# Performance work log

Hardware: AMD Instinct MI355X
Metric: run time of the kernel (lower is better)

The kernel has to match this reference:

```python
import jax, jax.numpy as jnp
import numpy as np

# dims
B, C, H, W = 2, 256, 128, 256
P, G = 9, 8            # num_pts, num_groups
GC = C // G            # group_channels


def setup_inputs() -> dict:
    key = jax.random.key(0)
    ks = jax.random.split(key, 8)
    s = 0.02
    return {
        "feats1": jax.random.normal(ks[0], (B, C, H, W), jnp.float32),
        "feats2": jax.random.normal(ks[1], (B, C, H, W), jnp.float32),
        "anchor_points": jax.random.uniform(ks[2], (B, H * W, 2), jnp.float32),
        "norm1_g": jnp.ones((C,), jnp.float32), "norm1_b": jnp.zeros((C,), jnp.float32),
        "norm2_g": jnp.ones((C,), jnp.float32), "norm2_b": jnp.zeros((C,), jnp.float32),
        "Wv": jax.random.normal(ks[3], (C, C), jnp.float32) * s, "bv": jnp.zeros((C,), jnp.float32),
        "Ww": jax.random.normal(ks[4], (C, G * P), jnp.float32) * s, "bw": jnp.zeros((G * P,), jnp.float32),
        "Wk": jax.random.normal(ks[5], (C, P), jnp.float32) * s, "bk": jnp.zeros((P,), jnp.float32),
        "Wo": jax.random.normal(ks[6], (C, C), jnp.float32) * s, "bo": jnp.zeros((C,), jnp.float32),
    }


def _ln(x, g, b):
    # LayerNorm over the last (channel) axis, eps as torch default
    m = jnp.mean(x, axis=-1, keepdims=True)
    v = jnp.mean(jnp.square(x - m), axis=-1, keepdims=True)
    return (x - m) * jax.lax.rsqrt(v + 1e-5) * g + b


def _bilinear_sample(value, pts):
    # value: (b, H, W, C); pts: (b, N, 2) normalized [0,1] (x, y)
    # grid_sample semantics: align_corners=False, zero padding
    b, h, w, c = value.shape
    x = pts[..., 0] * w - 0.5
    y = pts[..., 1] * h - 0.5
    x0 = jnp.floor(x)
    y0 = jnp.floor(y)
    wx = (x - x0)[..., None]
    wy = (y - y0)[..., None]
    x0i = x0.astype(jnp.int32)
    y0i = y0.astype(jnp.int32)
    vflat = value.reshape(b, h * w, c)

    def gather(yi, xi):
        valid = (yi >= 0) & (yi < h) & (xi >= 0) & (xi < w)
        idx = jnp.clip(yi, 0, h - 1) * w + jnp.clip(xi, 0, w - 1)
        g = jnp.take_along_axis(vflat, idx[..., None], axis=1)
        return g * valid[..., None].astype(value.dtype)

    v00 = gather(y0i, x0i)
    v01 = gather(y0i, x0i + 1)
    v10 = gather(y0i + 1, x0i)
    v11 = gather(y0i + 1, x0i + 1)
    return (v00 * (1 - wx) * (1 - wy) + v01 * wx * (1 - wy)
            + v10 * (1 - wx) * wy + v11 * wx * wy)


def reference(feats1, feats2, anchor_points, norm1_g, norm1_b, norm2_g, norm2_b,
              Wv, bv, Ww, bw, Wk, bk, Wo, bo):
    b, c, h, w = feats1.shape
    hw = h * w
    # to_3d(dim=2): (b, c, h, w) -> (b, hw, c); LayerNorm over c
    x1 = _ln(feats1.reshape(b, c, hw).transpose(0, 2, 1), norm1_g, norm1_b)
    x2 = _ln(feats2.reshape(b, c, hw).transpose(0, 2, 1), norm2_g, norm2_b)

    # value_proj (1x1 conv == per-pixel linear)
    value = (x2 @ Wv + bv).reshape(b, h, w, c)

    # weight_proj -> (b, hw, P, G); channel layout p*G + g; softmax over the P points per group
    logits = (x1 @ Ww + bw).reshape(b, hw, P, G)
    wts = jax.nn.softmax(logits, axis=2)

    # 1D key-point generator: per-pixel learned offsets along x around the anchor
    off = x1 @ Wk + bk                                   # (b, hw, P) normalized offsets
    kx = anchor_points[..., 0:1] + off                   # (b, hw, P)
    ky = jnp.broadcast_to(anchor_points[..., 1:2], kx.shape)
    kp = jnp.stack([kx, ky], axis=-1)                    # (b, hw, P, 2)

    # deformable aggregation: bilinear gather + group-weighted sum over points
    samp = _bilinear_sample(value, kp.reshape(b, hw * P, 2)).reshape(b, hw, P, G, GC)
    agg = jnp.einsum('bnpgc,bnpg->bngc', samp, wts).reshape(b, hw, c)

    out = (agg @ Wo + bo).reshape(b, h, w, c).transpose(0, 3, 1, 2)  # (b, c, h, w)
    return out, kp.reshape(b, h, w, P, 2)
```

## Files before the change

### kernel.cpp

```cpp
#include <hip/hip_runtime.h>
#include <hip/hip_bf16.h>


constexpr int B = 2, C = 256, H = 128, W = 256;
constexpr int HW = H * W;
constexpr int P = 9, G = 8;
constexpr int PIX = 32;
constexpr int NPIX = B * HW;
constexpr int NBKT = 2 * 129;

typedef __attribute__((ext_vector_type(8))) __bf16 bf16x8;
typedef __attribute__((ext_vector_type(4))) float f32x4;
typedef __attribute__((ext_vector_type(2))) float f32x2;
typedef __attribute__((ext_vector_type(2))) __fp16 fp16x2;

static __device__ __forceinline__ unsigned short f2bf(float x) {
    __hip_bfloat16 h = __float2bfloat16(x);
    return *reinterpret_cast<unsigned short*>(&h);
}
static __device__ __forceinline__ unsigned int pack2(float a, float b) {
    return (unsigned int)f2bf(a) | ((unsigned int)f2bf(b) << 16);
}
static __device__ __forceinline__ unsigned int pkh(float a, float b) {
    fp16x2 h = __builtin_amdgcn_cvt_pkrtz(a, b);
    return *reinterpret_cast<unsigned int*>(&h);
}
static __device__ __forceinline__ float bf2f(unsigned short u) {
    return __uint_as_float((unsigned int)u << 16);
}
static __device__ __forceinline__ bf16x8 ldb8g(const unsigned short* p) {
    return *reinterpret_cast<const bf16x8*>(p);
}

#define FMA_LO(acc, pk, c) \
    asm("v_fma_mix_f32 %0, %1, %2, %0 op_sel:[0,0,0] op_sel_hi:[1,0,0]" \
        : "+v"(acc) : "v"(pk), "v"(c))
#define FMA_HI(acc, pk, c) \
    asm("v_fma_mix_f32 %0, %1, %2, %0 op_sel:[1,0,0] op_sel_hi:[1,0,0]" \
        : "+v"(acc) : "v"(pk), "v"(c))

__global__ __launch_bounds__(256) void k_prep(
    const float* __restrict__ Ww, const float* __restrict__ Wv,
    const float* __restrict__ Wo,
    unsigned short* __restrict__ WwT, unsigned short* __restrict__ WvT,
    unsigned short* __restrict__ WoT)
{
    int tid = blockIdx.x * 256 + threadIdx.x;
    if (tid < 20480) {
        int n = tid >> 8, k = tid & 255;
        WwT[tid] = f2bf((n < 72) ? Ww[k * 72 + n] : 0.f);
    } else if (tid < 20480 + 65536) {
        int i = tid - 20480;
        int n = i >> 8, k = i & 255;
        WvT[i] = f2bf(Wv[k * 256 + n]);
    } else {
        int i = tid - 86016;
        int n = i >> 8, k = i & 255;
        WoT[i] = f2bf(Wo[k * 256 + n]);
    }
}

static __device__ __forceinline__ int bucket_of(const float* anchor, int pix) {
    float ay = anchor[(size_t)pix * 2 + 1];
    int y0 = (int)floorf(ay * (float)H - 0.5f);
    y0 = min(max(y0, -1), H - 1);
    return (pix >> 15) * 129 + y0 + 1;
}

__global__ __launch_bounds__(1024) void k_hist(
    const float* __restrict__ anchor, int* __restrict__ hist64)
{
    __shared__ int h[NBKT];
    const int t = threadIdx.x, blk = blockIdx.x;
    for (int i = t; i < NBKT; i += 1024) h[i] = 0;
    __syncthreads();
    atomicAdd(&h[bucket_of(anchor, blk * 1024 + t)], 1);
    __syncthreads();
    for (int i = t; i < NBKT; i += 1024) hist64[blk * NBKT + i] = h[i];
}

__global__ __launch_bounds__(256) void k_scan(
    const int* __restrict__ hist64, int* __restrict__ off)
{
    __shared__ int tot[NBKT], base[NBKT];
    const int t = threadIdx.x;
    for (int bkt = t; bkt < NBKT; bkt += 256) {
        int run = 0;
        for (int blk = 0; blk < 64; ++blk) run += hist64[blk * NBKT + bkt];
        tot[bkt] = run;
    }
    __syncthreads();
    if (t == 0) {
        int run = 0;
        for (int i = 0; i < NBKT; ++i) { base[i] = run; run += tot[i]; }
    }
    __syncthreads();
    for (int bkt = t; bkt < NBKT; bkt += 256) {
        int run = base[bkt];
        for (int blk = 0; blk < 64; ++blk) {
            int v = hist64[blk * NBKT + bkt];
            off[blk * NBKT + bkt] = run;
            run += v;
        }
    }
}

__global__ __launch_bounds__(1024) void k_scatter(
    const float* __restrict__ anchor, const int* __restrict__ off,
    int* __restrict__ perm)
{
    __shared__ int cur[NBKT];
    const int t = threadIdx.x, blk = blockIdx.x;
    for (int i = t; i < NBKT; i += 1024) cur[i] = off[blk * NBKT + i];
    __syncthreads();
    int pix = blk * 1024 + t;
    int pos = atomicAdd(&cur[bucket_of(anchor, pix)], 1);
    perm[pos] = pix;
}

__global__ __launch_bounds__(256) void kA(
    const float* __restrict__ feats1, const float* __restrict__ anchor,
    const float* __restrict__ g1, const float* __restrict__ b1,
    const float* __restrict__ Wk, const float* __restrict__ bk,
    const unsigned short* __restrict__ WwT, const float* __restrict__ bw,
    unsigned short* __restrict__ wtsb, float* __restrict__ kp_out)
{
    __shared__ __align__(16) char uXH[32768];
    __shared__ __align__(16) char smB[20480];
    __shared__ float meanA[PIX], rstdA[PIX], axL[PIX], ayL[PIX];

    float* Xt = (float*)uXH;
    unsigned short (*Hi)[264] = reinterpret_cast<unsigned short(*)[264]>(uXH);

    float* WkL  = (float*)smB;
    float* red2 = (float*)(smB + 9216);
    float* red  = (float*)(smB + 18432);
    float* Lg   = (float*)smB;

    const int t = threadIdx.x;
    const int p = t & 31;
    const int part = t >> 5;
    const int gpix0 = blockIdx.x * PIX;
    const int b = gpix0 >> 15;
    const int n0 = gpix0 & (HW - 1);
    const float* Fb = feats1 + (size_t)b * C * HW;

    for (int i = t; i < 2304; i += 256) WkL[i] = Wk[i];
    if (t < PIX) {
        axL[t] = anchor[((size_t)gpix0 + t) * 2 + 0];
        ayL[t] = anchor[((size_t)gpix0 + t) * 2 + 1];
    }

    {
        const int sr = t >> 3;
        const int sc = (t & 7) * 4;
        #pragma unroll
        for (int i = 0; i < 8; ++i) {
            int row = sr + 32 * i;
            float4 v = *reinterpret_cast<const float4*>(
                Fb + (size_t)row * HW + n0 + sc);
            *reinterpret_cast<float4*>(&Xt[row * 32 + sc]) = v;
        }
    }
    __syncthreads();

    float x[32];
    #pragma unroll
    for (int i = 0; i < 32; ++i)
        x[i] = Xt[(part * 32 + i) * 32 + p];

    float s = 0.f, ss = 0.f;
    #pragma unroll
    for (int i = 0; i < 32; ++i) { s += x[i]; ss += x[i] * x[i]; }
    red[part * 32 + p] = s;
    red[256 + part * 32 + p] = ss;
    __syncthreads();
    if (part == 0) {
        float s2 = 0.f, ss2 = 0.f;
        #pragma unroll
        for (int k = 0; k < 8; ++k) { s2 += red[k * 32 + p]; ss2 += red[256 + k * 32 + p]; }
        float mean = s2 * (1.f / C);
        float var  = ss2 * (1.f / C) - mean * mean;
        meanA[p] = mean; rstdA[p] = rsqrtf(var + 1e-5f);
    }
    __syncthreads();

    {
        float mean = meanA[p], rstd = rstdA[p];
        #pragma unroll
        for (int i = 0; i < 32; ++i) {
            int c = part * 32 + i;
            x[i] = (x[i] - mean) * rstd * g1[c] + b1[c];
        }
    }

    {
        float po[9];
        #pragma unroll
        for (int pt = 0; pt < 9; ++pt) po[pt] = 0.f;
        #pragma unroll 4
        for (int i = 0; i < 32; ++i) {
            int c = part * 32 + i;
            float xv = x[i];
            #pragma unroll
            for (int pt = 0; pt < 9; ++pt) po[pt] += xv * WkL[c * 9 + pt];
        }
        #pragma unroll
        for (int pt = 0; pt < 9; ++pt) red2[(part * 32 + p) * 9 + pt] = po[pt];
    }

    {
        unsigned int* row = (unsigned int*)&Hi[p][part * 32];
        #pragma unroll
        for (int i = 0; i < 16; ++i) row[i] = pack2(x[2 * i], x[2 * i + 1]);
    }
    __syncthreads();

    for (int tau = t; tau < 288; tau += 256) {
        int px = tau & 31, pt = tau >> 5;
        float offv = bk[pt];
        #pragma unroll
        for (int k = 0; k < 8; ++k) offv += red2[(k * 32 + px) * 9 + pt];
        size_t o = (((size_t)gpix0 + px) * P + pt) * 2;
        kp_out[o] = axL[px] + offv;
        kp_out[o + 1] = ayL[px];
    }

    const int wave = t >> 6, lane = t & 63;
    const int l15 = lane & 15, quad = lane >> 4;
    const int mt = wave & 1;
    const int ntb = (wave >> 1) * 3;
    const int ntc = (wave >> 1) ? 2 : 3;

    f32x4 acc[3];
    #pragma unroll
    for (int j = 0; j < 3; ++j) acc[j] = (f32x4){0.f, 0.f, 0.f, 0.f};

    const unsigned short* arow = &Hi[mt * 16 + l15][quad * 8];
    for (int kk = 0; kk < 8; ++kk) {
        bf16x8 a = *reinterpret_cast<const bf16x8*>(arow + kk * 32);
        for (int j = 0; j < 3; ++j) {
            if (j < ntc) {
                bf16x8 bfr = ldb8g(WwT + (size_t)((ntb + j) * 16 + l15) * 256 + quad * 8 + kk * 32);
                acc[j] = __builtin_amdgcn_mfma_f32_16x16x32_bf16(a, bfr, acc[j], 0, 0, 0);
            }
        }
    }
    __syncthreads();

    #pragma unroll
    for (int j = 0; j < 3; ++j) {
        if (j < ntc) {
            int n = (ntb + j) * 16 + l15;
            if (n < 72) {
                float bwn = bw[n];
                #pragma unroll
                for (int r = 0; r < 4; ++r)
                    Lg[(mt * 16 + quad * 4 + r) * 81 + n] = acc[j][r] + bwn;
            }
        }
    }
    __syncthreads();

    {
        int px = t >> 3, g = t & 7;
        float m = -1e30f;
        #pragma unroll
        for (int pt = 0; pt < P; ++pt) m = fmaxf(m, Lg[px * 81 + pt * 8 + g]);
        float e[P], sum = 0.f;
        #pragma unroll
        for (int pt = 0; pt < P; ++pt) { e[pt] = __expf(Lg[px * 81 + pt * 8 + g] - m); sum += e[pt]; }
        float inv = 1.f / sum;
        unsigned short* wb = wtsb + ((size_t)gpix0 + px) * 72 + g * 9;
        #pragma unroll
        for (int pt = 0; pt < P; ++pt) wb[pt] = f2bf(e[pt] * inv);
    }
}

__global__ __launch_bounds__(256) void kB(
    const float* __restrict__ feats2,
    const float* __restrict__ g2, const float* __restrict__ b2,
    const unsigned short* __restrict__ WvT, const float* __restrict__ bv,
    unsigned short* __restrict__ val)
{
    __shared__ __align__(16) char uXH[32768];
    __shared__ float red[2][8][PIX];
    __shared__ float meanA[PIX], rstdA[PIX];

    float* Xt = (float*)uXH;
    unsigned short (*Hi)[264] = reinterpret_cast<unsigned short(*)[264]>(uXH);

    const int t = threadIdx.x;
    const int p = t & 31;
    const int part = t >> 5;
    const int gpix0 = blockIdx.x * PIX;
    const int b = gpix0 >> 15;
    const int n0 = gpix0 & (HW - 1);
    const float* Fb = feats2 + (size_t)b * C * HW;

    {
        const int sr = t >> 3;
        const int sc = (t & 7) * 4;
        #pragma unroll
        for (int i = 0; i < 8; ++i) {
            int row = sr + 32 * i;
            float4 v = *reinterpret_cast<const float4*>(
                Fb + (size_t)row * HW + n0 + sc);
            *reinterpret_cast<float4*>(&Xt[row * 32 + sc]) = v;
        }
    }
    __syncthreads();

    float x[32];
    #pragma unroll
    for (int i = 0; i < 32; ++i)
        x[i] = Xt[(part * 32 + i) * 32 + p];

    float s = 0.f, ss = 0.f;
    #pragma unroll
    for (int i = 0; i < 32; ++i) { s += x[i]; ss += x[i] * x[i]; }
    red[0][part][p] = s; red[1][part][p] = ss;
    __syncthreads();
    if (part == 0) {
        float s2 = 0.f, ss2 = 0.f;
        #pragma unroll
        for (int k = 0; k < 8; ++k) { s2 += red[0][k][p]; ss2 += red[1][k][p]; }
        float mean = s2 * (1.f / C);
        float var  = ss2 * (1.f / C) - mean * mean;
        meanA[p] = mean; rstdA[p] = rsqrtf(var + 1e-5f);
    }
    __syncthreads();
    {
        float mean = meanA[p], rstd = rstdA[p];
        unsigned int* row = (unsigned int*)&Hi[p][part * 32];
        #pragma unroll
        for (int i = 0; i < 16; ++i) {
            float v0 = (x[2 * i] - mean) * rstd * g2[part * 32 + 2 * i] + b2[part * 32 + 2 * i];
            float v1 = (x[2 * i + 1] - mean) * rstd * g2[part * 32 + 2 * i + 1] + b2[part * 32 + 2 * i + 1];
            row[i] = pack2(v0, v1);
        }
    }
    __syncthreads();

    const int wave = t >> 6, lane = t & 63;
    const int l15 = lane & 15, quad = lane >> 4;
    const int m0 = wave * 64;

    f32x4 acc[4][2];
    #pragma unroll
    for (int ms = 0; ms < 4; ++ms)
        #pragma unroll
        for (int nt = 0; nt < 2; ++nt)
            acc[ms][nt] = (f32x4){0.f, 0.f, 0.f, 0.f};

    for (int kk = 0; kk < 8; ++kk) {
        bf16x8 a[4], bfr[2];
        #pragma unroll
        for (int ms = 0; ms < 4; ++ms)
            a[ms] = ldb8g(WvT + (size_t)(m0 + ms * 16 + l15) * 256 + quad * 8 + kk * 32);
        #pragma unroll
        for (int nt = 0; nt < 2; ++nt)
            bfr[nt] = *reinterpret_cast<const bf16x8*>(&Hi[nt * 16 + l15][quad * 8 + kk * 32]);
        #pragma unroll
        for (int ms = 0; ms < 4; ++ms)
            #pragma unroll
            for (int nt = 0; nt < 2; ++nt)
                acc[ms][nt] = __builtin_amdgcn_mfma_f32_16x16x32_bf16(a[ms], bfr[nt], acc[ms][nt], 0, 0, 0);
    }

    #pragma unroll
    for (int ms = 0; ms < 4; ++ms) {
        int ch0 = m0 + ms * 16 + quad * 4;
        float b0 = bv[ch0], b1v = bv[ch0 + 1], b2v = bv[ch0 + 2], b3 = bv[ch0 + 3];
        #pragma unroll
        for (int nt = 0; nt < 2; ++nt) {
            int pix = gpix0 + nt * 16 + l15;
            uint2 o;
            o.x = pkh(acc[ms][nt][0] + b0, acc[ms][nt][1] + b1v);
            o.y = pkh(acc[ms][nt][2] + b2v, acc[ms][nt][3] + b3);
            *reinterpret_cast<uint2*>(val + (size_t)pix * 256 + ch0) = o;
        }
    }
}

template <int PTBASE, int NPT>
static __device__ __forceinline__ void issue_loads(
    uint2* q, int cw, const char* pr0, const char* pr1, unsigned lane8)
{
    #pragma unroll
    for (int j = 0; j < NPT; ++j) {
        unsigned xb0 = (unsigned)__builtin_amdgcn_readlane(cw, (PTBASE + j) * 6 + 4);
        unsigned xb1 = (unsigned)__builtin_amdgcn_readlane(cw, (PTBASE + j) * 6 + 5);
        q[4 * j + 0] = *(const uint2*)(pr0 + xb0 + lane8);
        q[4 * j + 1] = *(const uint2*)(pr0 + xb1 + lane8);
        q[4 * j + 2] = *(const uint2*)(pr1 + xb0 + lane8);
        q[4 * j + 3] = *(const uint2*)(pr1 + xb1 + lane8);
    }
}

template <int PTBASE, int NPT>
static __device__ __forceinline__ void fma_block(
    const uint2* q, int cw, const float* wl,
    float& a0, float& a1, float& a2, float& a3)
{
    #pragma unroll
    for (int j = 0; j < NPT; ++j) {
        const int pt = PTBASE + j;
        float u00 = __int_as_float(__builtin_amdgcn_readlane(cw, pt * 6 + 0));
        float u01 = __int_as_float(__builtin_amdgcn_readlane(cw, pt * 6 + 1));
        float u10 = __int_as_float(__builtin_amdgcn_readlane(cw, pt * 6 + 2));
        float u11 = __int_as_float(__builtin_amdgcn_readlane(cw, pt * 6 + 3));
        float w = wl[pt];
        float c00 = w * u00, c01 = w * u01, c10 = w * u10, c11 = w * u11;

        FMA_LO(a0, q[4 * j + 0].x, c00); FMA_HI(a1, q[4 * j + 0].x, c00);
        FMA_LO(a2, q[4 * j + 0].y, c00); FMA_HI(a3, q[4 * j + 0].y, c00);
        FMA_LO(a0, q[4 * j + 1].x, c01); FMA_HI(a1, q[4 * j + 1].x, c01);
        FMA_LO(a2, q[4 * j + 1].y, c01); FMA_HI(a3, q[4 * j + 1].y, c01);
        FMA_LO(a0, q[4 * j + 2].x, c10); FMA_HI(a1, q[4 * j + 2].x, c10);
        FMA_LO(a2, q[4 * j + 2].y, c10); FMA_HI(a3, q[4 * j + 2].y, c10);
        FMA_LO(a0, q[4 * j + 3].x, c11); FMA_HI(a1, q[4 * j + 3].x, c11);
        FMA_LO(a2, q[4 * j + 3].y, c11); FMA_HI(a3, q[4 * j + 3].y, c11);
    }
}

__global__ __launch_bounds__(256, 4) void k_gather(
    const unsigned short* __restrict__ wtsb,
    const float* __restrict__ kp,
    const unsigned short* __restrict__ val,
    const int* __restrict__ perm,
    unsigned short* __restrict__ aggb)
{
    __shared__ int   CF[PIX][66];
    __shared__ float WL[PIX * 8 * 11];
    __shared__ float EY[PIX][2];
    __shared__ int pixL[PIX];

    const int t = threadIdx.x;
    const int phys = blockIdx.x;
    const int lb = (phys & 7) * 256 + (phys >> 3);
    const int gpix0 = lb * PIX;

    if (t < PIX) {
        int pix = perm[gpix0 + t];
        pixL[t] = pix;
        float ay = kp[(size_t)pix * 18 + 1];
        float yf = ay * (float)H - 0.5f;
        float y0f = floorf(yf);
        float wy = yf - y0f;
        int y0 = (int)y0f;
        EY[t][0] = (((unsigned)y0 < (unsigned)H) ? 1.f : 0.f) * (1.f - wy);
        EY[t][1] = (((unsigned)(y0 + 1) < (unsigned)H) ? 1.f : 0.f) * wy;
        int yb0 = min(max(y0, 0), H - 1) * W;
        int yb1 = min(max(y0 + 1, 0), H - 1) * W;
        int base = (pix >> 15) * HW;
        CF[t][54] = (base + yb0) << 9;
        CF[t][55] = (base + yb1) << 9;
    }
    __syncthreads();

    for (int tau = t; tau < 288; tau += 256) {
        int px = tau & 31, pt = tau >> 5;
        int pix = pixL[px];
        float kx = kp[(size_t)pix * 18 + 2 * pt];
        float e0 = EY[px][0], e1 = EY[px][1];
        float xf = kx * (float)W - 0.5f;
        float x0f = floorf(xf);
        float wx = xf - x0f;
        int x0 = (int)x0f;
        float g0 = (1.f - wx) * (((unsigned)x0 < (unsigned)W) ? 1.f : 0.f);
        float g1v = wx * (((unsigned)(x0 + 1) < (unsigned)W) ? 1.f : 0.f);
        CF[px][pt * 6 + 0] = __float_as_int(g0 * e0);
        CF[px][pt * 6 + 1] = __float_as_int(g1v * e0);
        CF[px][pt * 6 + 2] = __float_as_int(g0 * e1);
        CF[px][pt * 6 + 3] = __float_as_int(g1v * e1);
        CF[px][pt * 6 + 4] = min(max(x0, 0), W - 1) << 9;
        CF[px][pt * 6 + 5] = min(max(x0 + 1, 0), W - 1) << 9;
    }
    {
        int px = t >> 3, j = t & 7;
        int pix = pixL[px];
        const unsigned short* wrow = wtsb + (size_t)pix * 72 + j * 9;
        float* wl = &WL[(px * 8 + j) * 11];
        #pragma unroll
        for (int k = 0; k < 9; ++k) wl[k] = bf2f(wrow[k]);
    }
    __syncthreads();

    const int wave = t >> 6, lane = t & 63;
    const int gl = lane >> 3;
    const char* vb = (const char*)val;
    const unsigned lane8 = (unsigned)lane * 8u;

    uint2 qa[16], qb[20];

    int px = wave;
    int cwA = CF[px][lane];
    {
        unsigned rb0 = (unsigned)__builtin_amdgcn_readlane(cwA, 54);
        unsigned rb1 = (unsigned)__builtin_amdgcn_readlane(cwA, 55);
        const char* pr0 = vb + rb0;
        const char* pr1 = vb + rb1;
        issue_loads<0, 4>(qa, cwA, pr0, pr1, lane8);
    }
    unsigned rbA0 = (unsigned)__builtin_amdgcn_readlane(cwA, 54);
    unsigned rbA1 = (unsigned)__builtin_amdgcn_readlane(cwA, 55);

    for (int i = 0; i < 8; ++i) {
        const float* wl = &WL[(px * 8 + gl) * 11];
        const char* pr0A = vb + rbA0;
        const char* pr1A = vb + rbA1;

        issue_loads<4, 5>(qb, cwA, pr0A, pr1A, lane8);
        __builtin_amdgcn_sched_barrier(0);

        float a0 = 0.f, a1 = 0.f, a2 = 0.f, a3 = 0.f;
        fma_block<0, 4>(qa, cwA, wl, a0, a1, a2, a3);

        int pxn = (i < 7) ? px + 4 : px;
        int cwN = CF[pxn][lane];
        unsigned rbN0 = (unsigned)__builtin_amdgcn_readlane(cwN, 54);
        unsigned rbN1 = (unsigned)__builtin_amdgcn_readlane(cwN, 55);
        {
            const char* pr0N = vb + rbN0;
            const char* pr1N = vb + rbN1;
            issue_loads<0, 4>(qa, cwN, pr0N, pr1N, lane8);
        }
        __builtin_amdgcn_sched_barrier(0);

        fma_block<4, 5>(qb, cwA, wl, a0, a1, a2, a3);

        int pix = pixL[px];
        uint2 o;
        o.x = pack2(a0, a1);
        o.y = pack2(a2, a3);
        *reinterpret_cast<uint2*>(aggb + ((size_t)pix << 8) + 4 * lane) = o;

        cwA = cwN; rbA0 = rbN0; rbA1 = rbN1; px = pxn;
    }
}

__global__ __launch_bounds__(256) void k_gemmo(
    const unsigned short* __restrict__ aggb,
    const unsigned short* __restrict__ WoT,
    const float* __restrict__ bo,
    float* __restrict__ out)
{
    const int t = threadIdx.x;
    const int wave = t >> 6, lane = t & 63;
    const int n_base = blockIdx.x * 64;
    const int b = n_base >> 15;
    const int hw0 = n_base & (HW - 1);
    const int m0 = wave * 64;
    const int l15 = lane & 15, quad = lane >> 4;

    f32x4 acc[4][4];
    #pragma unroll
    for (int ms = 0; ms < 4; ++ms)
        #pragma unroll
        for (int ns = 0; ns < 4; ++ns)
            acc[ms][ns] = (f32x4){0.f, 0.f, 0.f, 0.f};

    size_t aoff[4], boff[4];
    #pragma unroll
    for (int ms = 0; ms < 4; ++ms)
        aoff[ms] = (size_t)(m0 + ms * 16 + l15) * 256 + quad * 8;
    #pragma unroll
    for (int ns = 0; ns < 4; ++ns)
        boff[ns] = (size_t)(n_base + ns * 16 + l15) * 256 + quad * 8;

    for (int kk = 0; kk < 8; ++kk) {
        bf16x8 a[4], bfr[4];
        #pragma unroll
        for (int ms = 0; ms < 4; ++ms) a[ms] = ldb8g(WoT + aoff[ms] + kk * 32);
        #pragma unroll
        for (int ns = 0; ns < 4; ++ns) bfr[ns] = ldb8g(aggb + boff[ns] + kk * 32);
        #pragma unroll
        for (int ms = 0; ms < 4; ++ms)
            #pragma unroll
            for (int ns = 0; ns < 4; ++ns)
                acc[ms][ns] = __builtin_amdgcn_mfma_f32_16x16x32_bf16(a[ms], bfr[ns], acc[ms][ns], 0, 0, 0);
    }

    float bor[4][4];
    #pragma unroll
    for (int ms = 0; ms < 4; ++ms)
        #pragma unroll
        for (int r = 0; r < 4; ++r)
            bor[ms][r] = bo[m0 + ms * 16 + quad * 4 + r];

    #pragma unroll
    for (int ms = 0; ms < 4; ++ms) {
        #pragma unroll
        for (int ns = 0; ns < 4; ++ns) {
            #pragma unroll
            for (int r = 0; r < 4; ++r) {
                int ch = m0 + ms * 16 + quad * 4 + r;
                out[((size_t)b * 256 + ch) * HW + hw0 + ns * 16 + l15] = acc[ms][ns][r] + bor[ms][r];
            }
        }
    }
}

extern "C" void kernel_launch(void* const* d_in, const int* in_sizes, int n_in,
                              void* d_out, int out_size, void* d_ws, size_t ws_size,
                              hipStream_t stream)
{
    const float* feats1 = (const float*)d_in[0];
    const float* feats2 = (const float*)d_in[1];
    const float* anchor = (const float*)d_in[2];
    const float* n1g    = (const float*)d_in[3];
    const float* n1b    = (const float*)d_in[4];
    const float* n2g    = (const float*)d_in[5];
    const float* n2b    = (const float*)d_in[6];
    const float* Wv     = (const float*)d_in[7];
    const float* bv     = (const float*)d_in[8];
    const float* Ww     = (const float*)d_in[9];
    const float* bw     = (const float*)d_in[10];
    const float* Wk     = (const float*)d_in[11];
    const float* bk     = (const float*)d_in[12];
    const float* Wo     = (const float*)d_in[13];
    const float* bo     = (const float*)d_in[14];

    float* out = (float*)d_out;
    float* kp  = out + (size_t)B * C * HW;

    char* ws = (char*)d_ws;
    unsigned short* val  = (unsigned short*)(ws);
    unsigned short* aggb = (unsigned short*)(ws + 33554432);
    unsigned short* wtsb = (unsigned short*)(ws + 67108864);
    unsigned short* WwT  = (unsigned short*)(ws + 76546048);
    unsigned short* WvT  = (unsigned short*)(ws + 76587008);
    unsigned short* WoT  = (unsigned short*)(ws + 76718080);
    int* perm   = (int*)(ws + 76849152);
    int* hist64 = (int*)(ws + 77111296);
    int* off    = (int*)(ws + 77375488);

    k_prep   <<<592,  256,  0, stream>>>(Ww, Wv, Wo, WwT, WvT, WoT);
    k_hist   <<<64,   1024, 0, stream>>>(anchor, hist64);
    k_scan   <<<1,    256,  0, stream>>>(hist64, off);
    k_scatter<<<64,   1024, 0, stream>>>(anchor, off, perm);
    kA       <<<2048, 256,  0, stream>>>(feats1, anchor, n1g, n1b, Wk, bk, WwT, bw, wtsb, kp);
    kB       <<<2048, 256,  0, stream>>>(feats2, n2g, n2b, WvT, bv, val);
    k_gather <<<2048, 256,  0, stream>>>(wtsb, kp, val, perm, aggb);
    k_gemmo  <<<1024, 256,  0, stream>>>(aggb, WoT, bo, out);
}
```

Measured before the change: 397.3 us.

## Stage kernel outputs through shared memory for coalesced vector stores; parallelize bucket scan

Several kernels (kA key-point and softmax-weight outputs, kB value outputs, k_gemmo final output) now write results into LDS first and then copy them out with wide, contiguous 16-byte global stores, replacing scattered narrow per-lane writes. k_scan replaces a single-thread serial prefix sum over the buckets with a parallel Hillis-Steele scan in shared memory. The goal is fewer, better-coalesced global write transactions and less serial work. The cost is extra LDS usage and additional __syncthreads barriers, which may reduce occupancy.

Result: no change. 394.2 us (-0.8%).

```diff
diff --git a/kernel.cpp b/kernel.cpp
--- a/kernel.cpp
+++ b/kernel.cpp
@@ -82,7 +82,8 @@
 __global__ __launch_bounds__(256) void k_scan(
     const int* __restrict__ hist64, int* __restrict__ off)
 {
-    __shared__ int tot[NBKT], base[NBKT];
+    __shared__ int tot[NBKT];
+    __shared__ int sc[512];
     const int t = threadIdx.x;
     for (int bkt = t; bkt < NBKT; bkt += 256) {
         int run = 0;
@@ -90,13 +91,19 @@
         tot[bkt] = run;
     }
     __syncthreads();
-    if (t == 0) {
-        int run = 0;
-        for (int i = 0; i < NBKT; ++i) { base[i] = run; run += tot[i]; }
-    }
-    __syncthreads();
+    sc[t] = (t < NBKT) ? tot[t] : 0;
+    sc[t + 256] = (t + 256 < NBKT) ? tot[t + 256] : 0;
+    __syncthreads();
+    for (int s = 1; s < 512; s <<= 1) {
+        int a0 = (t >= s) ? sc[t - s] : 0;
+        int a1 = (t + 256 >= s) ? sc[t + 256 - s] : 0;
+        __syncthreads();
+        sc[t] += a0;
+        sc[t + 256] += a1;
+        __syncthreads();
+    }
     for (int bkt = t; bkt < NBKT; bkt += 256) {
-        int run = base[bkt];
+        int run = (bkt > 0) ? sc[bkt - 1] : 0;
         for (int blk = 0; blk < 64; ++blk) {
             int v = hist64[blk * NBKT + bkt];
             off[blk * NBKT + bkt] = run;
@@ -127,10 +134,13 @@
 {
     __shared__ __align__(16) char uXH[32768];
     __shared__ __align__(16) char smB[20480];
+    __shared__ __align__(16) char uKW[4608];
     __shared__ float meanA[PIX], rstdA[PIX], axL[PIX], ayL[PIX];
 
     float* Xt = (float*)uXH;
     unsigned short (*Hi)[264] = reinterpret_cast<unsigned short(*)[264]>(uXH);
+    float* kpL = (float*)uKW;
+    unsigned short* wtsL = (unsigned short*)uKW;
 
     float* WkL  = (float*)smB;
     float* red2 = (float*)(smB + 9216);
@@ -221,9 +231,8 @@
         float offv = bk[pt];
         #pragma unroll
         for (int k = 0; k < 8; ++k) offv += red2[(k * 32 + px) * 9 + pt];
-        size_t o = (((size_t)gpix0 + px) * P + pt) * 2;
-        kp_out[o] = axL[px] + offv;
-        kp_out[o + 1] = ayL[px];
+        kpL[px * 18 + pt * 2]     = axL[px] + offv;
+        kpL[px * 18 + pt * 2 + 1] = ayL[px];
     }
 
     const int wave = t >> 6, lane = t & 63;
@@ -247,6 +256,11 @@
         }
     }
     __syncthreads();
+
+    if (t < 144) {
+        float4 v = *reinterpret_cast<const float4*>(&kpL[t * 4]);
+        *reinterpret_cast<float4*>(kp_out + (size_t)gpix0 * 18 + t * 4) = v;
+    }
 
     #pragma unroll
     for (int j = 0; j < 3; ++j) {
@@ -271,9 +285,16 @@
         #pragma unroll
         for (int pt = 0; pt < P; ++pt) { e[pt] = __expf(Lg[px * 81 + pt * 8 + g] - m); sum += e[pt]; }
         float inv = 1.f / sum;
-        unsigned short* wb = wtsb + ((size_t)gpix0 + px) * 72 + g * 9;
-        #pragma unroll
-        for (int pt = 0; pt < P; ++pt) wb[pt] = f2bf(e[pt] * inv);
+        #pragma unroll
+        for (int pt = 0; pt < P; ++pt) wtsL[px * 72 + g * 9 + pt] = f2bf(e[pt] * inv);
+    }
+    __syncthreads();
+
+    {
+        const uint4* sw = (const uint4*)wtsL;
+        uint4* dw = (uint4*)(wtsb + (size_t)gpix0 * 72);
+        dw[t] = sw[t];
+        if (t < 32) dw[256 + t] = sw[256 + t];
     }
 }
 
@@ -289,6 +310,7 @@
 
     float* Xt = (float*)uXH;
     unsigned short (*Hi)[264] = reinterpret_cast<unsigned short(*)[264]>(uXH);
+    unsigned int* vt = (unsigned int*)uXH;
 
     const int t = threadIdx.x;
     const int p = t & 31;
@@ -367,6 +389,7 @@
             for (int nt = 0; nt < 2; ++nt)
                 acc[ms][nt] = __builtin_amdgcn_mfma_f32_16x16x32_bf16(a[ms], bfr[nt], acc[ms][nt], 0, 0, 0);
     }
+    __syncthreads();
 
     #pragma unroll
     for (int ms = 0; ms < 4; ++ms) {
@@ -374,11 +397,24 @@
         float b0 = bv[ch0], b1v = bv[ch0 + 1], b2v = bv[ch0 + 2], b3 = bv[ch0 + 3];
         #pragma unroll
         for (int nt = 0; nt < 2; ++nt) {
-            int pix = gpix0 + nt * 16 + l15;
+            int px = nt * 16 + l15;
             uint2 o;
             o.x = pkh(acc[ms][nt][0] + b0, acc[ms][nt][1] + b1v);
             o.y = pkh(acc[ms][nt][2] + b2v, acc[ms][nt][3] + b3);
-            *reinterpret_cast<uint2*>(val + (size_t)pix * 256 + ch0) = o;
+            *reinterpret_cast<uint2*>(&vt[px * 132 + (ch0 >> 1)]) = o;
+        }
+    }
+    __syncthreads();
+
+    {
+        const int px = t >> 3, j = t & 7;
+        unsigned int* dst = (unsigned int*)(val + (size_t)(gpix0 + px) * 256);
+        const unsigned int* srcr = &vt[px * 132];
+        #pragma unroll
+        for (int k = 0; k < 4; ++k) {
+            int u = j * 4 + k * 32;
+            uint4 v = *reinterpret_cast<const uint4*>(&srcr[u]);
+            *reinterpret_cast<uint4*>(&dst[u]) = v;
         }
     }
 }
@@ -546,6 +582,8 @@
     const float* __restrict__ bo,
     float* __restrict__ out)
 {
+    __shared__ __align__(16) float Ot[256 * 33];
+
     const int t = threadIdx.x;
     const int wave = t >> 6, lane = t & 63;
     const int n_base = blockIdx.x * 64;
@@ -590,14 +628,28 @@
             bor[ms][r] = bo[m0 + ms * 16 + quad * 4 + r];
 
     #pragma unroll
-    for (int ms = 0; ms < 4; ++ms) {
-        #pragma unroll
-        for (int ns = 0; ns < 4; ++ns) {
+    for (int h = 0; h < 2; ++h) {
+        if (h) __syncthreads();
+        #pragma unroll
+        for (int ms = 0; ms < 4; ++ms) {
             #pragma unroll
-            for (int r = 0; r < 4; ++r) {
-                int ch = m0 + ms * 16 + quad * 4 + r;
-                out[((size_t)b * 256 + ch) * HW + hw0 + ns * 16 + l15] = acc[ms][ns][r] + bor[ms][r];
+            for (int nn = 0; nn < 2; ++nn) {
+                const int ns = 2 * h + nn;
+                #pragma unroll
+                for (int r = 0; r < 4; ++r) {
+                    int ch = m0 + ms * 16 + quad * 4 + r;
+                    Ot[ch * 33 + nn * 16 + l15] = acc[ms][ns][r] + bor[ms][r];
+                }
             }
+        }
+        __syncthreads();
+        #pragma unroll
+        for (int it = 0; it < 8; ++it) {
+            int ch = it * 32 + (t >> 3);
+            const float* src = &Ot[ch * 33 + (t & 7) * 4];
+            float4 v = {src[0], src[1], src[2], src[3]};
+            *reinterpret_cast<float4*>(
+                out + ((size_t)b * 256 + ch) * HW + hw0 + h * 32 + (t & 7) * 4) = v;
         }
     }
 }
```
